# Performance work log

Hardware: AMD Instinct MI355X
Metric: run time of the kernel (lower is better)

The kernel has to match this reference:

```python
import jax, jax.numpy as jnp
import numpy as np

C = 256
HEADS = 8
HD = C // HEADS
EPS = 1e-5


def _layernorm(x, g, b):
    mu = jnp.mean(x, axis=-1, keepdims=True)
    var = jnp.var(x, axis=-1, keepdims=True)
    return (x - mu) * jax.lax.rsqrt(var + EPS) * g + b


def setup_inputs() -> dict:
    key = jax.random.key(0)
    ks = jax.random.split(key, 16)
    s = 0.02
    return {
        "x": jax.random.normal(ks[0], (1, C, 64, 64), jnp.float32),
        "bn_gamma": 1.0 + s * jax.random.normal(ks[1], (C,), jnp.float32),
        "bn_beta": s * jax.random.normal(ks[2], (C,), jnp.float32),
        "bn_mean": s * jax.random.normal(ks[3], (C,), jnp.float32),
        "bn_var": jnp.ones((C,), jnp.float32),
        "w_in": s * jax.random.normal(ks[4], (C, C), jnp.float32),
        "b_in": jnp.zeros((C,), jnp.float32),
        "ln1_g": jnp.ones((C,), jnp.float32),
        "ln1_b": jnp.zeros((C,), jnp.float32),
        "w_qkv": s * jax.random.normal(ks[5], (3 * C, C), jnp.float32),
        "b_qkv": jnp.zeros((3 * C,), jnp.float32),
        "w_ap": s * jax.random.normal(ks[6], (C, C), jnp.float32),
        "b_ap": jnp.zeros((C,), jnp.float32),
        "ln2_g": jnp.ones((C,), jnp.float32),
        "ln2_b": jnp.zeros((C,), jnp.float32),
        "w_ff1": s * jax.random.normal(ks[7], (4 * C, C), jnp.float32),
        "b_ff1": jnp.zeros((4 * C,), jnp.float32),
        "w_ff2": s * jax.random.normal(ks[8], (C, 4 * C), jnp.float32),
        "b_ff2": jnp.zeros((C,), jnp.float32),
        "w_out": s * jax.random.normal(ks[9], (C, C), jnp.float32),
        "b_out": jnp.zeros((C,), jnp.float32),
    }


def reference(x, bn_gamma, bn_beta, bn_mean, bn_var, w_in, b_in,
              ln1_g, ln1_b, w_qkv, b_qkv, w_ap, b_ap,
              ln2_g, ln2_b, w_ff1, b_ff1, w_ff2, b_ff2, w_out, b_out):
    b, c, h, w = x.shape
    t = h * w
    x_in = x
    # BatchNorm2d (eval mode: running stats)
    xn = (x - bn_mean[None, :, None, None]) * jax.lax.rsqrt(bn_var + EPS)[None, :, None, None]
    xn = xn * bn_gamma[None, :, None, None] + bn_beta[None, :, None, None]
    # proj_in 1x1 conv -> tokens [b, t, c]
    tok = xn.reshape(b, c, t).transpose(0, 2, 1)
    tok = tok @ w_in.T + b_in
    # transformer block (depth=1)
    y = _layernorm(tok, ln1_g, ln1_b)  # norm1
    qkv = y @ w_qkv.T + b_qkv  # [b, t, 3c], channel split (3, H, hd)
    qkv = qkv.reshape(b, t, 3, HEADS, HD)
    q = qkv[:, :, 0].transpose(0, 2, 1, 3)  # [b, H, t, hd]
    k = qkv[:, :, 1].transpose(0, 2, 1, 3)
    v = qkv[:, :, 2].transpose(0, 2, 1, 3)
    scale = HD ** (-0.5)
    attn = jax.nn.softmax(jnp.einsum('bhqd,bhkd->bhqk', q, k) * scale, axis=-1)
    o = jnp.einsum('bhqk,bhkd->bhqd', attn, v)  # [b, H, t, hd]
    o = o.transpose(0, 2, 1, 3).reshape(b, t, c)  # channels ordered (H, hd)
    o = o @ w_ap.T + b_ap  # attn proj 1x1
    attn_out = o + y  # VanillaAttention residual adds its (normed) input
    tok = tok + attn_out
    # FFN
    z = _layernorm(tok, ln2_g, ln2_b)
    z = jax.nn.gelu(z @ w_ff1.T + b_ff1, approximate=False)
    tok = tok + (z @ w_ff2.T + b_ff2)
    # back to image, proj_out 1x1, outer residual
    x4 = tok.transpose(0, 2, 1).reshape(b, c, h, w)
    out = jnp.einsum('oc,bchw->bohw', w_out, x4) + b_out[None, :, None, None]
    return out + x_in
```

## Files before the change

### kernel.cpp

```cpp
#include <hip/hip_runtime.h>
#include <math.h>

#define T_TOK 4096
#define C_DIM 256
#define EPSF  1e-5f
#define SC_QL (0.17677669529663687f * 1.4426950408889634f)

typedef short  bf16x8  __attribute__((ext_vector_type(8)));
typedef float  f32x4   __attribute__((ext_vector_type(4)));
typedef ushort ushort8 __attribute__((ext_vector_type(8)));

__device__ __forceinline__ short f2bf(float f) {
    unsigned u = __builtin_bit_cast(unsigned, f);
    unsigned r = (u + 0x7FFFu + ((u >> 16) & 1u)) >> 16;
    return (short)r;
}
__device__ __forceinline__ float bf2f(ushort u) {
    return __builtin_bit_cast(float, ((unsigned)u) << 16);
}
__device__ __forceinline__ unsigned pk_bf16(float a, float b) {
    const unsigned ua = __builtin_bit_cast(unsigned, a) + 0x8000u;
    const unsigned ub = __builtin_bit_cast(unsigned, b) + 0x8000u;
    return __builtin_amdgcn_perm(ub, ua, 0x07060302u);
}
template <int CTRL>
__device__ __forceinline__ float dppf(float x) {
    return __builtin_bit_cast(float,
        __builtin_amdgcn_mov_dpp(__builtin_bit_cast(int, x), CTRL, 0xF, 0xF, true));
}
__device__ __forceinline__ float rowsum16(float x) {
    x += dppf<0xB1>(x);
    x += dppf<0x4E>(x);
    x += dppf<0x141>(x);
    x += dppf<0x140>(x);
    return x;
}
#define MFMA16(a, b, c) __builtin_amdgcn_mfma_f32_16x16x32_bf16(a, b, c, 0, 0, 0)

__global__ __launch_bounds__(256) void prep_kernel(
    const float* __restrict__ w_in, const float* __restrict__ w_qkv,
    const float* __restrict__ w_ap, const float* __restrict__ w_ff1,
    const float* __restrict__ w_ff2, const float* __restrict__ w_out,
    const float* __restrict__ b_qkv, ushort* __restrict__ wbuf,
    float* __restrict__ bqs,
    const float* __restrict__ x, const float* __restrict__ gamma,
    const float* __restrict__ beta, const float* __restrict__ mean,
    const float* __restrict__ var, ushort* __restrict__ tin)
{
    __shared__ float tile[32][33];
    if (blockIdx.x < 896) {
        const int gid = blockIdx.x * 256 + threadIdx.x;
        const int e0 = gid * 4;
        const float* src; int off; float sc = 1.f;
        if (e0 < 65536)       { src = w_in;  off = e0; }
        else if (e0 < 262144) { src = w_qkv; off = e0 - 65536; if (off < 65536) sc = SC_QL; }
        else if (e0 < 327680) { src = w_ap;  off = e0 - 262144; }
        else if (e0 < 589824) { src = w_ff1; off = e0 - 327680; }
        else if (e0 < 851968) { src = w_ff2; off = e0 - 589824; }
        else                  { src = w_out; off = e0 - 851968; }
        const float4 v = *(const float4*)(src + off);
        ushort4 o;
        o.x = (ushort)f2bf(v.x * sc); o.y = (ushort)f2bf(v.y * sc);
        o.z = (ushort)f2bf(v.z * sc); o.w = (ushort)f2bf(v.w * sc);
        *(ushort4*)(wbuf + e0) = o;
        if (gid < 192) {
            const float s2 = (gid < 64) ? SC_QL : 1.f;
            float4 b = ((const float4*)b_qkv)[gid];
            b.x *= s2; b.y *= s2; b.z *= s2; b.w *= s2;
            ((float4*)bqs)[gid] = b;
        }
    } else {
        const int bidx = blockIdx.x - 896;
        const int t0 = (bidx & 127) * 32, c0 = (bidx >> 7) * 32;
        const int tx = threadIdx.x & 31, ty = threadIdx.x >> 5;
#pragma unroll
        for (int i = 0; i < 32; i += 8) {
            const int c = c0 + ty + i;
            const float a = rsqrtf(var[c] + EPSF) * gamma[c];
            const float d = beta[c] - mean[c] * a;
            tile[ty + i][tx] = x[c * T_TOK + t0 + tx] * a + d;
        }
        __syncthreads();
#pragma unroll
        for (int i = 0; i < 32; i += 8) {
            const int t = t0 + ty + i;
            tin[t * C_DIM + c0 + tx] = (ushort)f2bf(tile[tx][ty + i]);
        }
    }
}

__global__ __launch_bounds__(1024) void fused_pre(
    const ushort* __restrict__ tin, const ushort* __restrict__ wb_in,
    const float* __restrict__ b_in, const float* __restrict__ ln1_g,
    const float* __restrict__ ln1_b, const ushort* __restrict__ wb_qkv,
    const float* __restrict__ bqs, float* __restrict__ tok0,
    float* __restrict__ yout, ushort* __restrict__ qkvb)
{
    __shared__ ushort Atile[16 * 264];
    __shared__ ushort Ytile[16 * 264];
    __shared__ float  red[16][16][2];
    const int t0 = blockIdx.x * 16;
    const int tid = threadIdx.x, wv = tid >> 6, lane = tid & 63;
    const int c = lane & 15, g = lane >> 4;

    {
        const int r = tid >> 6, c0 = (tid & 63) * 4;
        *(ushort4*)&Atile[r * 264 + c0] = *(const ushort4*)(tin + (size_t)(t0 + r) * 256 + c0);
    }
    __syncthreads();

    f32x4 accp = {};
#pragma unroll
    for (int kc = 0; kc < 8; ++kc) {
        const bf16x8 af = *(const bf16x8*)&Atile[c * 264 + kc * 32 + g * 8];
        const bf16x8 bfv = *(const bf16x8*)(wb_in +
            (size_t)(wv * 16 + c) * 256 + kc * 32 + g * 8);
        accp = MFMA16(af, bfv, accp);
    }
    const int colp = wv * 16 + c;
    {
        const float bb = b_in[colp];
        float vs[4], s1[4], s2[4];
#pragma unroll
        for (int rr = 0; rr < 4; ++rr) {
            const float v = accp[rr] + bb;
            vs[rr] = v; s1[rr] = v; s2[rr] = v * v;
            tok0[(size_t)(t0 + 4 * g + rr) * 256 + colp] = v;
        }
#pragma unroll
        for (int rr = 0; rr < 4; ++rr) { s1[rr] = rowsum16(s1[rr]); s2[rr] = rowsum16(s2[rr]); }
        if (c == 0) {
#pragma unroll
            for (int rr = 0; rr < 4; ++rr) {
                red[wv][4 * g + rr][0] = s1[rr];
                red[wv][4 * g + rr][1] = s2[rr];
            }
        }
        __syncthreads();
        if (tid < 32) {
            const int row = tid >> 1, j = tid & 1;
            float s = 0.f;
#pragma unroll
            for (int w = 0; w < 16; ++w) s += red[w][row][j];
            red[0][row][j] = s;
        }
        __syncthreads();
        const float gg = ln1_g[colp], lb = ln1_b[colp];
#pragma unroll
        for (int rr = 0; rr < 4; ++rr) {
            const int row = 4 * g + rr;
            const float mu = red[0][row][0] * (1.0f / 256.0f);
            const float var = red[0][row][1] * (1.0f / 256.0f) - mu * mu;
            const float rs = rsqrtf(var + EPSF);
            const float yv = (vs[rr] - mu) * rs * gg + lb;
            yout[(size_t)(t0 + row) * 256 + colp] = yv;
            Ytile[row * 264 + colp] = (ushort)f2bf(yv);
        }
    }
    __syncthreads();

    f32x4 accq[3] = {};
#pragma unroll
    for (int kc = 0; kc < 8; ++kc) {
        const bf16x8 af = *(const bf16x8*)&Ytile[c * 264 + kc * 32 + g * 8];
#pragma unroll
        for (int nf = 0; nf < 3; ++nf) {
            const bf16x8 bfv = *(const bf16x8*)(wb_qkv +
                (size_t)(wv * 48 + nf * 16 + c) * 256 + kc * 32 + g * 8);
            accq[nf] = MFMA16(af, bfv, accq[nf]);
        }
    }
#pragma unroll
    for (int nf = 0; nf < 3; ++nf) {
        const int col = wv * 48 + nf * 16 + c;
        const float bb = bqs[col];
#pragma unroll
        for (int rr = 0; rr < 4; ++rr)
            qkvb[(size_t)(t0 + 4 * g + rr) * 768 + col] = (ushort)f2bf(accq[nf][rr] + bb);
    }
}

#define KS   40
#define VTS  72
#define PS_W 36

__global__ __launch_bounds__(256) void attn_mfma(
    const ushort* __restrict__ qkv, ushort* __restrict__ o1,
    ushort* __restrict__ o2, float* __restrict__ lpart)
{
    const int h    = blockIdx.y;
    const int q0   = blockIdx.x << 6;
    const int half = blockIdx.z;
    const int tid  = threadIdx.x;
    const int wv   = tid >> 6, lane = tid & 63;
    const int c    = lane & 15, g = lane >> 4;

    __shared__ ushort Ks[2][64 * KS];
    __shared__ ushort Vt[2][32 * VTS];
    __shared__ float  Ps[4][16 * PS_W];

    const bf16x8 qf = *(const bf16x8*)(qkv + (size_t)(q0 + wv * 16 + c) * 768 + h * 32 + g * 8);

    bf16x8 ones;
#pragma unroll
    for (int i = 0; i < 8; ++i) ones[i] = (short)0x3F80;

    f32x4 oacc0 = {0.f, 0.f, 0.f, 0.f};
    f32x4 oacc1 = {0.f, 0.f, 0.f, 0.f};
    f32x4 oaccl = {0.f, 0.f, 0.f, 0.f};

    const int kr = tid >> 2, kc = (tid & 3) * 8;
    const int vp = tid & 31, vd = (tid >> 5) * 4;
    const ushort* kbase = qkv + 256 + h * 32;
    const ushort* vbase = qkv + 512 + h * 32;

    const int kt0 = half * 32, kt1 = kt0 + 32;
    ushort8 kpre  = *(const ushort8*)(kbase + ((size_t)kt0 * 64 + kr) * 768 + kc);
    ushort4 vpre0 = *(const ushort4*)(vbase + ((size_t)kt0 * 64 + 2 * vp) * 768 + vd);
    ushort4 vpre1 = *(const ushort4*)(vbase + ((size_t)kt0 * 64 + 2 * vp + 1) * 768 + vd);

    int p = 0;
    for (int kt = kt0; kt < kt1; ++kt) {
        *(ushort8*)&Ks[p][kr * KS + kc] = kpre;
        {
            unsigned* vtp = (unsigned*)&Vt[p][0];
            vtp[(vd + 0) * (VTS / 2) + vp] = (unsigned)vpre0.x | ((unsigned)vpre1.x << 16);
            vtp[(vd + 1) * (VTS / 2) + vp] = (unsigned)vpre0.y | ((unsigned)vpre1.y << 16);
            vtp[(vd + 2) * (VTS / 2) + vp] = (unsigned)vpre0.z | ((unsigned)vpre1.z << 16);
            vtp[(vd + 3) * (VTS / 2) + vp] = (unsigned)vpre0.w | ((unsigned)vpre1.w << 16);
        }
        __syncthreads();
        if (kt + 1 < kt1) {
            const size_t t0 = (size_t)(kt + 1) * 64;
            kpre  = *(const ushort8*)(kbase + (t0 + kr) * 768 + kc);
            vpre0 = *(const ushort4*)(vbase + (t0 + 2 * vp) * 768 + vd);
            vpre1 = *(const ushort4*)(vbase + (t0 + 2 * vp + 1) * 768 + vd);
        }

        const ushort* ks = &Ks[p][0];
        const ushort* vt = &Vt[p][0];
        const f32x4 zz = {0.f, 0.f, 0.f, 0.f};
        const bf16x8 k0 = *(const bf16x8*)&ks[(0 * 16 + c) * KS + g * 8];
        const bf16x8 k1 = *(const bf16x8*)&ks[(1 * 16 + c) * KS + g * 8];
        const bf16x8 k2 = *(const bf16x8*)&ks[(2 * 16 + c) * KS + g * 8];
        const bf16x8 k3 = *(const bf16x8*)&ks[(3 * 16 + c) * KS + g * 8];
        const f32x4 s0 = MFMA16(k0, qf, zz);
        const f32x4 s1 = MFMA16(k1, qf, zz);
        const f32x4 s2 = MFMA16(k2, qf, zz);
        const f32x4 s3 = MFMA16(k3, qf, zz);

        float* prow = &Ps[wv][c * PS_W];
        {
            const float e00 = __builtin_amdgcn_exp2f(s0[0]), e01 = __builtin_amdgcn_exp2f(s0[1]);
            const float e02 = __builtin_amdgcn_exp2f(s0[2]), e03 = __builtin_amdgcn_exp2f(s0[3]);
            const float e10 = __builtin_amdgcn_exp2f(s1[0]), e11 = __builtin_amdgcn_exp2f(s1[1]);
            const float e12 = __builtin_amdgcn_exp2f(s1[2]), e13 = __builtin_amdgcn_exp2f(s1[3]);
            const float e20 = __builtin_amdgcn_exp2f(s2[0]), e21 = __builtin_amdgcn_exp2f(s2[1]);
            const float e22 = __builtin_amdgcn_exp2f(s2[2]), e23 = __builtin_amdgcn_exp2f(s2[3]);
            const float e30 = __builtin_amdgcn_exp2f(s3[0]), e31 = __builtin_amdgcn_exp2f(s3[1]);
            const float e32 = __builtin_amdgcn_exp2f(s3[2]), e33 = __builtin_amdgcn_exp2f(s3[3]);
            prow[0 * 8 + 2 * g + 0] = __builtin_bit_cast(float, pk_bf16(e00, e01));
            prow[0 * 8 + 2 * g + 1] = __builtin_bit_cast(float, pk_bf16(e02, e03));
            prow[1 * 8 + 2 * g + 0] = __builtin_bit_cast(float, pk_bf16(e10, e11));
            prow[1 * 8 + 2 * g + 1] = __builtin_bit_cast(float, pk_bf16(e12, e13));
            prow[2 * 8 + 2 * g + 0] = __builtin_bit_cast(float, pk_bf16(e20, e21));
            prow[2 * 8 + 2 * g + 1] = __builtin_bit_cast(float, pk_bf16(e22, e23));
            prow[3 * 8 + 2 * g + 0] = __builtin_bit_cast(float, pk_bf16(e30, e31));
            prow[3 * 8 + 2 * g + 1] = __builtin_bit_cast(float, pk_bf16(e32, e33));
        }
#pragma unroll
        for (int ch = 0; ch < 2; ++ch) {
            const bf16x8 pf = *(const bf16x8*)&prow[ch * 16 + 4 * g];
            const bf16x8 v0 = *(const bf16x8*)&vt[(c)      * VTS + ch * 32 + g * 8];
            const bf16x8 v1 = *(const bf16x8*)&vt[(16 + c) * VTS + ch * 32 + g * 8];
            oacc0 = MFMA16(pf, v0, oacc0);
            oacc1 = MFMA16(pf, v1, oacc1);
            oaccl = MFMA16(pf, ones, oaccl);
        }
        p ^= 1;
        __syncthreads();
    }

    {
        ushort* op = (half ? o2 : o1) + (size_t)(q0 + wv * 16) * 256 + h * 32;
#pragma unroll
        for (int rr = 0; rr < 4; ++rr) {
            op[(4 * g + rr) * 256 + c]      = (ushort)f2bf(oacc0[rr]);
            op[(4 * g + rr) * 256 + 16 + c] = (ushort)f2bf(oacc1[rr]);
        }
        if (c == 0) {
#pragma unroll
            for (int rr = 0; rr < 4; ++rr)
                lpart[(size_t)(q0 + wv * 16 + 4 * g + rr) * 16 + half * 8 + h] = oaccl[rr];
        }
    }
}

__global__ __launch_bounds__(1024) void fused_mid(
    const ushort* __restrict__ o1, const ushort* __restrict__ o2,
    const float* __restrict__ lpart, const ushort* __restrict__ wb_ap,
    const float* __restrict__ b_ap, const float* __restrict__ yin,
    const float* __restrict__ tok0, const float* __restrict__ ln2_g,
    const float* __restrict__ ln2_b, const ushort* __restrict__ wb_ff1,
    const float* __restrict__ b_ff1, float* __restrict__ tok1,
    ushort* __restrict__ zbuf)
{
    __shared__ ushort Otile[16 * 264];
    __shared__ ushort Ztile[16 * 264];
    __shared__ float  red[16][16][2];
    const int t0 = blockIdx.x * 16;
    const int tid = threadIdx.x, wv = tid >> 6, lane = tid & 63;
    const int c = lane & 15, g = lane >> 4;

    {
        const int r = tid >> 6, c0 = (tid & 63) * 4;
        const int h = (tid & 63) >> 3;
        const float inv = 1.0f / (lpart[(size_t)(t0 + r) * 16 + h] +
                                  lpart[(size_t)(t0 + r) * 16 + 8 + h]);
        const ushort4 a = *(const ushort4*)(o1 + (size_t)(t0 + r) * 256 + c0);
        const ushort4 b = *(const ushort4*)(o2 + (size_t)(t0 + r) * 256 + c0);
        unsigned w[2];
        w[0] = pk_bf16((bf2f(a.x) + bf2f(b.x)) * inv, (bf2f(a.y) + bf2f(b.y)) * inv);
        w[1] = pk_bf16((bf2f(a.z) + bf2f(b.z)) * inv, (bf2f(a.w) + bf2f(b.w)) * inv);
        *(ushort4*)&Otile[r * 264 + c0] = *(ushort4*)w;
    }
    __syncthreads();

    f32x4 accp = {};
#pragma unroll
    for (int kc = 0; kc < 8; ++kc) {
        const bf16x8 af = *(const bf16x8*)&Otile[c * 264 + kc * 32 + g * 8];
        const bf16x8 bfv = *(const bf16x8*)(wb_ap +
            (size_t)(wv * 16 + c) * 256 + kc * 32 + g * 8);
        accp = MFMA16(af, bfv, accp);
    }
    const int colp = wv * 16 + c;
    {
        const float bb = b_ap[colp];
        float vs[4], s1[4], s2[4];
#pragma unroll
        for (int rr = 0; rr < 4; ++rr) {
            const size_t idx = (size_t)(t0 + 4 * g + rr) * 256 + colp;
            const float v = accp[rr] + bb + yin[idx] + tok0[idx];
            vs[rr] = v; s1[rr] = v; s2[rr] = v * v;
            tok1[idx] = v;
        }
#pragma unroll
        for (int rr = 0; rr < 4; ++rr) { s1[rr] = rowsum16(s1[rr]); s2[rr] = rowsum16(s2[rr]); }
        if (c == 0) {
#pragma unroll
            for (int rr = 0; rr < 4; ++rr) {
                red[wv][4 * g + rr][0] = s1[rr];
                red[wv][4 * g + rr][1] = s2[rr];
            }
        }
        __syncthreads();
        if (tid < 32) {
            const int row = tid >> 1, j = tid & 1;
            float s = 0.f;
#pragma unroll
            for (int w = 0; w < 16; ++w) s += red[w][row][j];
            red[0][row][j] = s;
        }
        __syncthreads();
        const float gg = ln2_g[colp], lb = ln2_b[colp];
#pragma unroll
        for (int rr = 0; rr < 4; ++rr) {
            const int row = 4 * g + rr;
            const float mu = red[0][row][0] * (1.0f / 256.0f);
            const float var = red[0][row][1] * (1.0f / 256.0f) - mu * mu;
            const float rs = rsqrtf(var + EPSF);
            const float zv = (vs[rr] - mu) * rs * gg + lb;
            Ztile[row * 264 + colp] = (ushort)f2bf(zv);
        }
    }
    __syncthreads();

    f32x4 accf[4] = {};
#pragma unroll
    for (int kc = 0; kc < 8; ++kc) {
        const bf16x8 af = *(const bf16x8*)&Ztile[c * 264 + kc * 32 + g * 8];
#pragma unroll
        for (int nf = 0; nf < 4; ++nf) {
            const bf16x8 bfv = *(const bf16x8*)(wb_ff1 +
                (size_t)(wv * 64 + nf * 16 + c) * 256 + kc * 32 + g * 8);
            accf[nf] = MFMA16(af, bfv, accf[nf]);
        }
    }
#pragma unroll
    for (int nf = 0; nf < 4; ++nf) {
        const int col = wv * 64 + nf * 16 + c;
        const float bb = b_ff1[col];
#pragma unroll
        for (int rr = 0; rr < 4; ++rr) {
            float v = accf[nf][rr] + bb;
            v = 0.5f * v * (1.0f + erff(v * 0.70710678118654752f));
            zbuf[(size_t)(t0 + 4 * g + rr) * 1024 + col] = (ushort)f2bf(v);
        }
    }
}

__global__ __launch_bounds__(1024) void fused_post(
    const ushort* __restrict__ zbuf, const ushort* __restrict__ wb_ff2,
    const float* __restrict__ b_ff2, const float* __restrict__ tok1,
    const ushort* __restrict__ wb_out, const float* __restrict__ b_out,
    const float* __restrict__ x, float* __restrict__ out)
{
    __shared__ ushort Ztile[16 * 1032];
    __shared__ ushort T2tile[16 * 264];
    const int t0 = blockIdx.x * 16;
    const int tid = threadIdx.x, wv = tid >> 6, lane = tid & 63;
    const int c = lane & 15, g = lane >> 4;

    {
        const int r = tid >> 6, c0 = (tid & 63) * 16;
        *(ushort8*)&Ztile[r * 1032 + c0] =
            *(const ushort8*)(zbuf + (size_t)(t0 + r) * 1024 + c0);
        *(ushort8*)&Ztile[r * 1032 + c0 + 8] =
            *(const ushort8*)(zbuf + (size_t)(t0 + r) * 1024 + c0 + 8);
    }
    __syncthreads();

    f32x4 accf = {};
#pragma unroll
    for (int kc = 0; kc < 32; ++kc) {
        const bf16x8 af = *(const bf16x8*)&Ztile[c * 1032 + kc * 32 + g * 8];
        const bf16x8 bfv = *(const bf16x8*)(wb_ff2 +
            (size_t)(wv * 16 + c) * 1024 + kc * 32 + g * 8);
        accf = MFMA16(af, bfv, accf);
    }
    {
        const int col = wv * 16 + c;
        const float bb = b_ff2[col];
#pragma unroll
        for (int rr = 0; rr < 4; ++rr) {
            const size_t idx = (size_t)(t0 + 4 * g + rr) * 256 + col;
            const float v = accf[rr] + bb + tok1[idx];
            T2tile[(4 * g + rr) * 264 + col] = (ushort)f2bf(v);
        }
    }
    __syncthreads();

    f32x4 acco = {};
#pragma unroll
    for (int kc = 0; kc < 8; ++kc) {
        const bf16x8 bfr = *(const bf16x8*)&T2tile[c * 264 + kc * 32 + g * 8];
        const bf16x8 afr = *(const bf16x8*)(wb_out +
            (size_t)(wv * 16 + c) * 256 + kc * 32 + g * 8);
        acco = MFMA16(afr, bfr, acco);
    }
#pragma unroll
    for (int rr = 0; rr < 4; ++rr) {
        const int och = wv * 16 + 4 * g + rr;
        const size_t idx = (size_t)och * T_TOK + t0 + c;
        out[idx] = acco[rr] + b_out[och] + x[idx];
    }
}

extern "C" void kernel_launch(void* const* d_in, const int* in_sizes, int n_in,
                              void* d_out, int out_size, void* d_ws, size_t ws_size,
                              hipStream_t stream)
{
    const float* x     = (const float*)d_in[0];
    const float* bn_g  = (const float*)d_in[1];
    const float* bn_b  = (const float*)d_in[2];
    const float* bn_m  = (const float*)d_in[3];
    const float* bn_v  = (const float*)d_in[4];
    const float* w_in  = (const float*)d_in[5];
    const float* b_in  = (const float*)d_in[6];
    const float* ln1_g = (const float*)d_in[7];
    const float* ln1_b = (const float*)d_in[8];
    const float* w_qkv = (const float*)d_in[9];
    const float* b_qkv = (const float*)d_in[10];
    const float* w_ap  = (const float*)d_in[11];
    const float* b_ap  = (const float*)d_in[12];
    const float* ln2_g = (const float*)d_in[13];
    const float* ln2_b = (const float*)d_in[14];
    const float* w_ff1 = (const float*)d_in[15];
    const float* b_ff1 = (const float*)d_in[16];
    const float* w_ff2 = (const float*)d_in[17];
    const float* b_ff2 = (const float*)d_in[18];
    const float* w_out = (const float*)d_in[19];
    const float* b_out = (const float*)d_in[20];
    float* out = (float*)d_out;
    float* ws  = (float*)d_ws;

    const size_t MF = 1u << 20;
    float*  tok0   = ws;
    float*  y      = ws + MF;
    float*  tok1   = ws + 2 * MF;
    ushort* qkv_bf = (ushort*)(ws + 3 * MF);
    ushort* zbuf   = (ushort*)(ws + 4 * MF + MF / 2);
    ushort* tin_bf = (ushort*)(ws + 6 * MF + MF / 2);
    ushort* o1p    = tin_bf;
    ushort* o2p    = (ushort*)(ws + 7 * MF);
    float*  lpart  = ws + 7 * MF + MF / 2;
    ushort* wbuf   = (ushort*)(ws + 7 * MF + MF / 2 + 65536);
    const ushort* wb_in  = wbuf;
    const ushort* wb_qkv = wbuf + 65536;
    const ushort* wb_ap  = wbuf + 262144;
    const ushort* wb_ff1 = wbuf + 327680;
    const ushort* wb_ff2 = wbuf + 589824;
    const ushort* wb_out = wbuf + 851968;
    float* bqs = (float*)(wbuf + 917504);

    prep_kernel<<<1920, 256, 0, stream>>>(w_in, w_qkv, w_ap, w_ff1, w_ff2, w_out,
                                          b_qkv, wbuf, bqs,
                                          x, bn_g, bn_b, bn_m, bn_v, tin_bf);
    fused_pre<<<256, 1024, 0, stream>>>(tin_bf, wb_in, b_in, ln1_g, ln1_b,
                                        wb_qkv, bqs, tok0, y, qkv_bf);
    attn_mfma<<<dim3(64, 8, 2), 256, 0, stream>>>(qkv_bf, o1p, o2p, lpart);
    fused_mid<<<256, 1024, 0, stream>>>(o1p, o2p, lpart, wb_ap, b_ap, y, tok0,
                                        ln2_g, ln2_b, wb_ff1, b_ff1, tok1, zbuf);
    fused_post<<<256, 1024, 0, stream>>>(zbuf, wb_ff2, b_ff2, tok1, wb_out, b_out,
                                         x, out);
}
```

Measured before the change: 204.8 us.

## Fold LayerNorm into weights, split attention keys four ways, preload weight fragments

LayerNorm gains are folded into the QKV and FF1 weights, and per-column u/d vectors are precomputed, so the matmuls run on the raw residual while mean and rstd are applied afterward. This lets the row-stat reduction overlap with the MFMA loop, and the y tensor is rebuilt from stored per-row stats instead of being written and re-read. Attention now splits the key range into four partitions instead of two for more parallelism, at the cost of more partial outputs to combine in fused_mid. Weight fragments are also preloaded into registers before the tile loads. Applying LayerNorm to unnormalized bf16 inputs carries some precision risk.

```diff
diff --git a/kernel.cpp b/kernel.cpp
--- a/kernel.cpp
+++ b/kernel.cpp
@@ -41,8 +41,10 @@
     const float* __restrict__ w_in, const float* __restrict__ w_qkv,
     const float* __restrict__ w_ap, const float* __restrict__ w_ff1,
     const float* __restrict__ w_ff2, const float* __restrict__ w_out,
-    const float* __restrict__ b_qkv, ushort* __restrict__ wbuf,
-    float* __restrict__ bqs,
+    const float* __restrict__ b_qkv, const float* __restrict__ b_ff1,
+    const float* __restrict__ ln1_g, const float* __restrict__ ln1_b,
+    const float* __restrict__ ln2_g, const float* __restrict__ ln2_b,
+    ushort* __restrict__ wbuf, float* __restrict__ u_all, float* __restrict__ d_all,
     const float* __restrict__ x, const float* __restrict__ gamma,
     const float* __restrict__ beta, const float* __restrict__ mean,
     const float* __restrict__ var, ushort* __restrict__ tin)
@@ -51,25 +53,28 @@
     if (blockIdx.x < 896) {
         const int gid = blockIdx.x * 256 + threadIdx.x;
         const int e0 = gid * 4;
-        const float* src; int off; float sc = 1.f;
+        const float* src; int off;
+        float4 sc = {1.f, 1.f, 1.f, 1.f};
         if (e0 < 65536)       { src = w_in;  off = e0; }
-        else if (e0 < 262144) { src = w_qkv; off = e0 - 65536; if (off < 65536) sc = SC_QL; }
+        else if (e0 < 262144) {
+            src = w_qkv; off = e0 - 65536;
+            const int k = off & 255;
+            sc = *(const float4*)(ln1_g + k);
+            if (off < 65536) { sc.x *= SC_QL; sc.y *= SC_QL; sc.z *= SC_QL; sc.w *= SC_QL; }
+        }
         else if (e0 < 327680) { src = w_ap;  off = e0 - 262144; }
-        else if (e0 < 589824) { src = w_ff1; off = e0 - 327680; }
+        else if (e0 < 589824) {
+            src = w_ff1; off = e0 - 327680;
+            sc = *(const float4*)(ln2_g + (off & 255));
+        }
         else if (e0 < 851968) { src = w_ff2; off = e0 - 589824; }
         else                  { src = w_out; off = e0 - 851968; }
         const float4 v = *(const float4*)(src + off);
         ushort4 o;
-        o.x = (ushort)f2bf(v.x * sc); o.y = (ushort)f2bf(v.y * sc);
-        o.z = (ushort)f2bf(v.z * sc); o.w = (ushort)f2bf(v.w * sc);
+        o.x = (ushort)f2bf(v.x * sc.x); o.y = (ushort)f2bf(v.y * sc.y);
+        o.z = (ushort)f2bf(v.z * sc.z); o.w = (ushort)f2bf(v.w * sc.w);
         *(ushort4*)(wbuf + e0) = o;
-        if (gid < 192) {
-            const float s2 = (gid < 64) ? SC_QL : 1.f;
-            float4 b = ((const float4*)b_qkv)[gid];
-            b.x *= s2; b.y *= s2; b.z *= s2; b.w *= s2;
-            ((float4*)bqs)[gid] = b;
-        }
-    } else {
+    } else if (blockIdx.x < 1920) {
         const int bidx = blockIdx.x - 896;
         const int t0 = (bidx & 127) * 32, c0 = (bidx >> 7) * 32;
         const int tx = threadIdx.x & 31, ty = threadIdx.x >> 5;
@@ -86,46 +91,76 @@
             const int t = t0 + ty + i;
             tin[t * C_DIM + c0 + tx] = (ushort)f2bf(tile[tx][ty + i]);
         }
+    } else {
+        const int row = (blockIdx.x - 1920) * 4 + (threadIdx.x >> 6);
+        const int lane = threadIdx.x & 63;
+        const float* W; const float* gv; const float* bv; float bias; float qs = 1.f;
+        if (row < 768) {
+            W = w_qkv + (size_t)row * 256; gv = ln1_g; bv = ln1_b; bias = b_qkv[row];
+            if (row < 256) qs = SC_QL;
+        } else {
+            const int r2 = row - 768;
+            W = w_ff1 + (size_t)r2 * 256; gv = ln2_g; bv = ln2_b; bias = b_ff1[r2];
+        }
+        const float4 w4 = *(const float4*)(W + lane * 4);
+        const float4 g4 = *(const float4*)(gv + lane * 4);
+        const float4 b4 = *(const float4*)(bv + lane * 4);
+        float su = w4.x * g4.x + w4.y * g4.y + w4.z * g4.z + w4.w * g4.w;
+        float sd = w4.x * b4.x + w4.y * b4.y + w4.z * b4.z + w4.w * b4.w;
+#pragma unroll
+        for (int off = 32; off > 0; off >>= 1) {
+            su += __shfl_xor(su, off);
+            sd += __shfl_xor(sd, off);
+        }
+        if (lane == 0) {
+            u_all[row] = qs * su;
+            d_all[row] = qs * (sd + bias);
+        }
     }
 }
 
 __global__ __launch_bounds__(1024) void fused_pre(
     const ushort* __restrict__ tin, const ushort* __restrict__ wb_in,
-    const float* __restrict__ b_in, const float* __restrict__ ln1_g,
-    const float* __restrict__ ln1_b, const ushort* __restrict__ wb_qkv,
-    const float* __restrict__ bqs, float* __restrict__ tok0,
-    float* __restrict__ yout, ushort* __restrict__ qkvb)
+    const float* __restrict__ b_in, const ushort* __restrict__ wb_qkv,
+    const float* __restrict__ u_all, const float* __restrict__ d_all,
+    float* __restrict__ tok0, float* __restrict__ lnstats,
+    ushort* __restrict__ qkvb)
 {
     __shared__ ushort Atile[16 * 264];
-    __shared__ ushort Ytile[16 * 264];
+    __shared__ ushort Vt[16 * 264];
     __shared__ float  red[16][16][2];
     const int t0 = blockIdx.x * 16;
     const int tid = threadIdx.x, wv = tid >> 6, lane = tid & 63;
     const int c = lane & 15, g = lane >> 4;
 
+    bf16x8 w1[8];
+#pragma unroll
+    for (int kc = 0; kc < 8; ++kc)
+        w1[kc] = *(const bf16x8*)(wb_in + (size_t)(wv * 16 + c) * 256 + kc * 32 + g * 8);
+
     {
         const int r = tid >> 6, c0 = (tid & 63) * 4;
         *(ushort4*)&Atile[r * 264 + c0] = *(const ushort4*)(tin + (size_t)(t0 + r) * 256 + c0);
     }
     __syncthreads();
 
-    f32x4 accp = {};
+    f32x4 acc1 = {};
 #pragma unroll
     for (int kc = 0; kc < 8; ++kc) {
         const bf16x8 af = *(const bf16x8*)&Atile[c * 264 + kc * 32 + g * 8];
-        const bf16x8 bfv = *(const bf16x8*)(wb_in +
-            (size_t)(wv * 16 + c) * 256 + kc * 32 + g * 8);
-        accp = MFMA16(af, bfv, accp);
+        acc1 = MFMA16(af, w1[kc], acc1);
     }
     const int colp = wv * 16 + c;
+    float vs[4];
     {
         const float bb = b_in[colp];
-        float vs[4], s1[4], s2[4];
-#pragma unroll
-        for (int rr = 0; rr < 4; ++rr) {
-            const float v = accp[rr] + bb;
+        float s1[4], s2[4];
+#pragma unroll
+        for (int rr = 0; rr < 4; ++rr) {
+            const float v = acc1[rr] + bb;
             vs[rr] = v; s1[rr] = v; s2[rr] = v * v;
             tok0[(size_t)(t0 + 4 * g + rr) * 256 + colp] = v;
+            Vt[(4 * g + rr) * 264 + colp] = (ushort)f2bf(v);
         }
 #pragma unroll
         for (int rr = 0; rr < 4; ++rr) { s1[rr] = rowsum16(s1[rr]); s2[rr] = rowsum16(s2[rr]); }
@@ -136,57 +171,64 @@
                 red[wv][4 * g + rr][1] = s2[rr];
             }
         }
-        __syncthreads();
-        if (tid < 32) {
-            const int row = tid >> 1, j = tid & 1;
-            float s = 0.f;
-#pragma unroll
-            for (int w = 0; w < 16; ++w) s += red[w][row][j];
-            red[0][row][j] = s;
-        }
-        __syncthreads();
-        const float gg = ln1_g[colp], lb = ln1_b[colp];
-#pragma unroll
-        for (int rr = 0; rr < 4; ++rr) {
-            const int row = 4 * g + rr;
-            const float mu = red[0][row][0] * (1.0f / 256.0f);
-            const float var = red[0][row][1] * (1.0f / 256.0f) - mu * mu;
-            const float rs = rsqrtf(var + EPSF);
-            const float yv = (vs[rr] - mu) * rs * gg + lb;
-            yout[(size_t)(t0 + row) * 256 + colp] = yv;
-            Ytile[row * 264 + colp] = (ushort)f2bf(yv);
-        }
-    }
-    __syncthreads();
-
-    f32x4 accq[3] = {};
+    }
+    __syncthreads();
+
+    if (tid < 32) {
+        const int row = tid >> 1, j = tid & 1;
+        float s = 0.f;
+#pragma unroll
+        for (int w = 0; w < 16; ++w) s += red[w][row][j];
+        red[0][row][j] = s;
+    }
+
+    f32x4 acc2[3] = {};
 #pragma unroll
     for (int kc = 0; kc < 8; ++kc) {
-        const bf16x8 af = *(const bf16x8*)&Ytile[c * 264 + kc * 32 + g * 8];
+        const bf16x8 af = *(const bf16x8*)&Vt[c * 264 + kc * 32 + g * 8];
 #pragma unroll
         for (int nf = 0; nf < 3; ++nf) {
             const bf16x8 bfv = *(const bf16x8*)(wb_qkv +
                 (size_t)(wv * 48 + nf * 16 + c) * 256 + kc * 32 + g * 8);
-            accq[nf] = MFMA16(af, bfv, accq[nf]);
+            acc2[nf] = MFMA16(af, bfv, acc2[nf]);
+        }
+    }
+    __syncthreads();
+
+    float mu[4], rs[4];
+#pragma unroll
+    for (int rr = 0; rr < 4; ++rr) {
+        const int row = 4 * g + rr;
+        mu[rr] = red[0][row][0] * (1.0f / 256.0f);
+        const float var = red[0][row][1] * (1.0f / 256.0f) - mu[rr] * mu[rr];
+        rs[rr] = rsqrtf(var + EPSF);
+    }
+    if (wv == 0 && c == 0) {
+#pragma unroll
+        for (int rr = 0; rr < 4; ++rr) {
+            lnstats[(size_t)(t0 + 4 * g + rr) * 2 + 0] = mu[rr];
+            lnstats[(size_t)(t0 + 4 * g + rr) * 2 + 1] = rs[rr];
         }
     }
 #pragma unroll
     for (int nf = 0; nf < 3; ++nf) {
         const int col = wv * 48 + nf * 16 + c;
-        const float bb = bqs[col];
-#pragma unroll
-        for (int rr = 0; rr < 4; ++rr)
-            qkvb[(size_t)(t0 + 4 * g + rr) * 768 + col] = (ushort)f2bf(accq[nf][rr] + bb);
+        const float u = u_all[col], d = d_all[col];
+#pragma unroll
+        for (int rr = 0; rr < 4; ++rr) {
+            const float q = rs[rr] * (acc2[nf][rr] - mu[rr] * u) + d;
+            qkvb[(size_t)(t0 + 4 * g + rr) * 768 + col] = (ushort)f2bf(q);
+        }
     }
 }
 
 #define KS   40
 #define VTS  72
-#define PS_W 36
+#define PS_W 34
 
 __global__ __launch_bounds__(256) void attn_mfma(
-    const ushort* __restrict__ qkv, ushort* __restrict__ o1,
-    ushort* __restrict__ o2, float* __restrict__ lpart)
+    const ushort* __restrict__ qkv, ushort* __restrict__ opart,
+    float* __restrict__ lpart)
 {
     const int h    = blockIdx.y;
     const int q0   = blockIdx.x << 6;
@@ -214,7 +256,7 @@
     const ushort* kbase = qkv + 256 + h * 32;
     const ushort* vbase = qkv + 512 + h * 32;
 
-    const int kt0 = half * 32, kt1 = kt0 + 32;
+    const int kt0 = half * 16, kt1 = kt0 + 16;
     ushort8 kpre  = *(const ushort8*)(kbase + ((size_t)kt0 * 64 + kr) * 768 + kc);
     ushort4 vpre0 = *(const ushort4*)(vbase + ((size_t)kt0 * 64 + 2 * vp) * 768 + vd);
     ushort4 vpre1 = *(const ushort4*)(vbase + ((size_t)kt0 * 64 + 2 * vp + 1) * 768 + vd);
@@ -270,7 +312,14 @@
         }
 #pragma unroll
         for (int ch = 0; ch < 2; ++ch) {
-            const bf16x8 pf = *(const bf16x8*)&prow[ch * 16 + 4 * g];
+            const float2 pA = *(const float2*)&prow[ch * 16 + 4 * g];
+            const float2 pB = *(const float2*)&prow[ch * 16 + 4 * g + 2];
+            unsigned pw[4];
+            pw[0] = __builtin_bit_cast(unsigned, pA.x);
+            pw[1] = __builtin_bit_cast(unsigned, pA.y);
+            pw[2] = __builtin_bit_cast(unsigned, pB.x);
+            pw[3] = __builtin_bit_cast(unsigned, pB.y);
+            const bf16x8 pf = *(const bf16x8*)pw;
             const bf16x8 v0 = *(const bf16x8*)&vt[(c)      * VTS + ch * 32 + g * 8];
             const bf16x8 v1 = *(const bf16x8*)&vt[(16 + c) * VTS + ch * 32 + g * 8];
             oacc0 = MFMA16(pf, v0, oacc0);
@@ -282,7 +331,7 @@
     }
 
     {
-        ushort* op = (half ? o2 : o1) + (size_t)(q0 + wv * 16) * 256 + h * 32;
+        ushort* op = opart + (size_t)half * (1u << 20) + (size_t)(q0 + wv * 16) * 256 + h * 32;
 #pragma unroll
         for (int rr = 0; rr < 4; ++rr) {
             op[(4 * g + rr) * 256 + c]      = (ushort)f2bf(oacc0[rr]);
@@ -291,59 +340,74 @@
         if (c == 0) {
 #pragma unroll
             for (int rr = 0; rr < 4; ++rr)
-                lpart[(size_t)(q0 + wv * 16 + 4 * g + rr) * 16 + half * 8 + h] = oaccl[rr];
+                lpart[(size_t)(q0 + wv * 16 + 4 * g + rr) * 32 + half * 8 + h] = oaccl[rr];
         }
     }
 }
 
 __global__ __launch_bounds__(1024) void fused_mid(
-    const ushort* __restrict__ o1, const ushort* __restrict__ o2,
-    const float* __restrict__ lpart, const ushort* __restrict__ wb_ap,
-    const float* __restrict__ b_ap, const float* __restrict__ yin,
-    const float* __restrict__ tok0, const float* __restrict__ ln2_g,
-    const float* __restrict__ ln2_b, const ushort* __restrict__ wb_ff1,
-    const float* __restrict__ b_ff1, float* __restrict__ tok1,
+    const ushort* __restrict__ opart, const float* __restrict__ lpart,
+    const ushort* __restrict__ wb_ap, const float* __restrict__ b_ap,
+    const float* __restrict__ tok0, const float* __restrict__ lnstats,
+    const float* __restrict__ ln1_g, const float* __restrict__ ln1_b,
+    const ushort* __restrict__ wb_ff1, const float* __restrict__ u_all,
+    const float* __restrict__ d_all, float* __restrict__ tok1,
     ushort* __restrict__ zbuf)
 {
     __shared__ ushort Otile[16 * 264];
-    __shared__ ushort Ztile[16 * 264];
+    __shared__ ushort Vt[16 * 264];
     __shared__ float  red[16][16][2];
     const int t0 = blockIdx.x * 16;
     const int tid = threadIdx.x, wv = tid >> 6, lane = tid & 63;
     const int c = lane & 15, g = lane >> 4;
 
+    bf16x8 w1[8];
+#pragma unroll
+    for (int kc = 0; kc < 8; ++kc)
+        w1[kc] = *(const bf16x8*)(wb_ap + (size_t)(wv * 16 + c) * 256 + kc * 32 + g * 8);
+
     {
         const int r = tid >> 6, c0 = (tid & 63) * 4;
         const int h = (tid & 63) >> 3;
-        const float inv = 1.0f / (lpart[(size_t)(t0 + r) * 16 + h] +
-                                  lpart[(size_t)(t0 + r) * 16 + 8 + h]);
-        const ushort4 a = *(const ushort4*)(o1 + (size_t)(t0 + r) * 256 + c0);
-        const ushort4 b = *(const ushort4*)(o2 + (size_t)(t0 + r) * 256 + c0);
+        const float* lp = lpart + (size_t)(t0 + r) * 32;
+        const float inv = 1.0f / (lp[h] + lp[8 + h] + lp[16 + h] + lp[24 + h]);
+        const size_t base = (size_t)(t0 + r) * 256 + c0;
+        const ushort4 a0 = *(const ushort4*)(opart + base);
+        const ushort4 a1 = *(const ushort4*)(opart + (1u << 20) + base);
+        const ushort4 a2 = *(const ushort4*)(opart + (2u << 20) + base);
+        const ushort4 a3 = *(const ushort4*)(opart + (3u << 20) + base);
         unsigned w[2];
-        w[0] = pk_bf16((bf2f(a.x) + bf2f(b.x)) * inv, (bf2f(a.y) + bf2f(b.y)) * inv);
-        w[1] = pk_bf16((bf2f(a.z) + bf2f(b.z)) * inv, (bf2f(a.w) + bf2f(b.w)) * inv);
+        w[0] = pk_bf16((bf2f(a0.x) + bf2f(a1.x) + bf2f(a2.x) + bf2f(a3.x)) * inv,
+                       (bf2f(a0.y) + bf2f(a1.y) + bf2f(a2.y) + bf2f(a3.y)) * inv);
+        w[1] = pk_bf16((bf2f(a0.z) + bf2f(a1.z) + bf2f(a2.z) + bf2f(a3.z)) * inv,
+                       (bf2f(a0.w) + bf2f(a1.w) + bf2f(a2.w) + bf2f(a3.w)) * inv);
         *(ushort4*)&Otile[r * 264 + c0] = *(ushort4*)w;
     }
     __syncthreads();
 
-    f32x4 accp = {};
+    f32x4 acc1 = {};
 #pragma unroll
     for (int kc = 0; kc < 8; ++kc) {
         const bf16x8 af = *(const bf16x8*)&Otile[c * 264 + kc * 32 + g * 8];
-        const bf16x8 bfv = *(const bf16x8*)(wb_ap +
-            (size_t)(wv * 16 + c) * 256 + kc * 32 + g * 8);
-        accp = MFMA16(af, bfv, accp);
+        acc1 = MFMA16(af, w1[kc], acc1);
     }
     const int colp = wv * 16 + c;
     {
         const float bb = b_ap[colp];
-        float vs[4], s1[4], s2[4];
-#pragma unroll
-        for (int rr = 0; rr < 4; ++rr) {
-            const size_t idx = (size_t)(t0 + 4 * g + rr) * 256 + colp;
-            const float v = accp[rr] + bb + yin[idx] + tok0[idx];
-            vs[rr] = v; s1[rr] = v; s2[rr] = v * v;
+        const float g1 = ln1_g[colp], b1 = ln1_b[colp];
+        float s1[4], s2[4];
+#pragma unroll
+        for (int rr = 0; rr < 4; ++rr) {
+            const int row = t0 + 4 * g + rr;
+            const size_t idx = (size_t)row * 256 + colp;
+            const float t0v = tok0[idx];
+            const float mu1 = lnstats[(size_t)row * 2 + 0];
+            const float rs1 = lnstats[(size_t)row * 2 + 1];
+            const float y = (t0v - mu1) * rs1 * g1 + b1;
+            const float v = acc1[rr] + bb + y + t0v;
+            s1[rr] = v; s2[rr] = v * v;
             tok1[idx] = v;
+            Vt[(4 * g + rr) * 264 + colp] = (ushort)f2bf(v);
         }
 #pragma unroll
         for (int rr = 0; rr < 4; ++rr) { s1[rr] = rowsum16(s1[rr]); s2[rr] = rowsum16(s2[rr]); }
@@ -354,46 +418,45 @@
                 red[wv][4 * g + rr][1] = s2[rr];
             }
         }
-        __syncthreads();
-        if (tid < 32) {
-            const int row = tid >> 1, j = tid & 1;
-            float s = 0.f;
-#pragma unroll
-            for (int w = 0; w < 16; ++w) s += red[w][row][j];
-            red[0][row][j] = s;
-        }
-        __syncthreads();
-        const float gg = ln2_g[colp], lb = ln2_b[colp];
-#pragma unroll
-        for (int rr = 0; rr < 4; ++rr) {
-            const int row = 4 * g + rr;
-            const float mu = red[0][row][0] * (1.0f / 256.0f);
-            const float var = red[0][row][1] * (1.0f / 256.0f) - mu * mu;
-            const float rs = rsqrtf(var + EPSF);
-            const float zv = (vs[rr] - mu) * rs * gg + lb;
-            Ztile[row * 264 + colp] = (ushort)f2bf(zv);
-        }
-    }
-    __syncthreads();
-
-    f32x4 accf[4] = {};
+    }
+    __syncthreads();
+
+    if (tid < 32) {
+        const int row = tid >> 1, j = tid & 1;
+        float s = 0.f;
+#pragma unroll
+        for (int w = 0; w < 16; ++w) s += red[w][row][j];
+        red[0][row][j] = s;
+    }
+
+    f32x4 acc2[4] = {};
 #pragma unroll
     for (int kc = 0; kc < 8; ++kc) {
-        const bf16x8 af = *(const bf16x8*)&Ztile[c * 264 + kc * 32 + g * 8];
+        const bf16x8 af = *(const bf16x8*)&Vt[c * 264 + kc * 32 + g * 8];
 #pragma unroll
         for (int nf = 0; nf < 4; ++nf) {
             const bf16x8 bfv = *(const bf16x8*)(wb_ff1 +
                 (size_t)(wv * 64 + nf * 16 + c) * 256 + kc * 32 + g * 8);
-            accf[nf] = MFMA16(af, bfv, accf[nf]);
-        }
+            acc2[nf] = MFMA16(af, bfv, acc2[nf]);
+        }
+    }
+    __syncthreads();
+
+    float mu[4], rs[4];
+#pragma unroll
+    for (int rr = 0; rr < 4; ++rr) {
+        const int row = 4 * g + rr;
+        mu[rr] = red[0][row][0] * (1.0f / 256.0f);
+        const float var = red[0][row][1] * (1.0f / 256.0f) - mu[rr] * mu[rr];
+        rs[rr] = rsqrtf(var + EPSF);
     }
 #pragma unroll
     for (int nf = 0; nf < 4; ++nf) {
         const int col = wv * 64 + nf * 16 + c;
-        const float bb = b_ff1[col];
-#pragma unroll
-        for (int rr = 0; rr < 4; ++rr) {
-            float v = accf[nf][rr] + bb;
+        const float u = u_all[768 + col], d = d_all[768 + col];
+#pragma unroll
+        for (int rr = 0; rr < 4; ++rr) {
+            float v = rs[rr] * (acc2[nf][rr] - mu[rr] * u) + d;
             v = 0.5f * v * (1.0f + erff(v * 0.70710678118654752f));
             zbuf[(size_t)(t0 + 4 * g + rr) * 1024 + col] = (ushort)f2bf(v);
         }
@@ -412,6 +475,11 @@
     const int tid = threadIdx.x, wv = tid >> 6, lane = tid & 63;
     const int c = lane & 15, g = lane >> 4;
 
+    bf16x8 w2[8];
+#pragma unroll
+    for (int kc = 0; kc < 8; ++kc)
+        w2[kc] = *(const bf16x8*)(wb_ff2 + (size_t)(wv * 16 + c) * 1024 + kc * 32 + g * 8);
+
     {
         const int r = tid >> 6, c0 = (tid & 63) * 16;
         *(ushort8*)&Ztile[r * 1032 + c0] =
@@ -423,7 +491,12 @@
 
     f32x4 accf = {};
 #pragma unroll
-    for (int kc = 0; kc < 32; ++kc) {
+    for (int kc = 0; kc < 8; ++kc) {
+        const bf16x8 af = *(const bf16x8*)&Ztile[c * 1032 + kc * 32 + g * 8];
+        accf = MFMA16(af, w2[kc], accf);
+    }
+#pragma unroll
+    for (int kc = 8; kc < 32; ++kc) {
         const bf16x8 af = *(const bf16x8*)&Ztile[c * 1032 + kc * 32 + g * 8];
         const bf16x8 bfv = *(const bf16x8*)(wb_ff2 +
             (size_t)(wv * 16 + c) * 1024 + kc * 32 + g * 8);
@@ -487,31 +560,34 @@
 
     const size_t MF = 1u << 20;
     float*  tok0   = ws;
-    float*  y      = ws + MF;
-    float*  tok1   = ws + 2 * MF;
+    float*  tok1   = ws + MF;
+    float*  lnst   = ws + 2 * MF;
     ushort* qkv_bf = (ushort*)(ws + 3 * MF);
-    ushort* zbuf   = (ushort*)(ws + 4 * MF + MF / 2);
-    ushort* tin_bf = (ushort*)(ws + 6 * MF + MF / 2);
-    ushort* o1p    = tin_bf;
-    ushort* o2p    = (ushort*)(ws + 7 * MF);
-    float*  lpart  = ws + 7 * MF + MF / 2;
-    ushort* wbuf   = (ushort*)(ws + 7 * MF + MF / 2 + 65536);
+    ushort* tin_bf = (ushort*)(ws + 4 * MF + MF / 2);
+    ushort* opart  = tin_bf;
+    ushort* zbuf   = (ushort*)(ws + 6 * MF + MF / 2);
+    float*  lpart  = ws + 8 * MF + MF / 2;
+    ushort* wbuf   = (ushort*)(ws + 8 * MF + MF / 2 + 131072);
     const ushort* wb_in  = wbuf;
     const ushort* wb_qkv = wbuf + 65536;
     const ushort* wb_ap  = wbuf + 262144;
     const ushort* wb_ff1 = wbuf + 327680;
     const ushort* wb_ff2 = wbuf + 589824;
     const ushort* wb_out = wbuf + 851968;
-    float* bqs = (float*)(wbuf + 917504);
-
-    prep_kernel<<<1920, 256, 0, stream>>>(w_in, w_qkv, w_ap, w_ff1, w_ff2, w_out,
-                                          b_qkv, wbuf, bqs,
-                                          x, bn_g, bn_b, bn_m, bn_v, tin_bf);
-    fused_pre<<<256, 1024, 0, stream>>>(tin_bf, wb_in, b_in, ln1_g, ln1_b,
-                                        wb_qkv, bqs, tok0, y, qkv_bf);
-    attn_mfma<<<dim3(64, 8, 2), 256, 0, stream>>>(qkv_bf, o1p, o2p, lpart);
-    fused_mid<<<256, 1024, 0, stream>>>(o1p, o2p, lpart, wb_ap, b_ap, y, tok0,
-                                        ln2_g, ln2_b, wb_ff1, b_ff1, tok1, zbuf);
+    float* u_all = (float*)(wbuf + 917504);
+    float* d_all = u_all + 1792;
+
+    prep_kernel<<<2368, 256, 0, stream>>>(
+        w_in, w_qkv, w_ap, w_ff1, w_ff2, w_out,
+        b_qkv, b_ff1, ln1_g, ln1_b, ln2_g, ln2_b,
+        wbuf, u_all, d_all,
+        x, bn_g, bn_b, bn_m, bn_v, tin_bf);
+    fused_pre<<<256, 1024, 0, stream>>>(tin_bf, wb_in, b_in, wb_qkv,
+                                        u_all, d_all, tok0, lnst, qkv_bf);
+    attn_mfma<<<dim3(64, 8, 4), 256, 0, stream>>>(qkv_bf, opart, lpart);
+    fused_mid<<<256, 1024, 0, stream>>>(opart, lpart, wb_ap, b_ap, tok0, lnst,
+                                        ln1_g, ln1_b, wb_ff1, u_all, d_all,
+                                        tok1, zbuf);
     fused_post<<<256, 1024, 0, stream>>>(zbuf, wb_ff2, b_ff2, tok1, wb_out, b_out,
                                          x, out);
 }
```

After: 205.0 us. No clear change (+0.1%).
